# Optimization experiments

Hardware: AMD Instinct MI355X
Metric: run time of the kernel (lower is better)

## Reference

```python
import jax, jax.numpy as jnp
import numpy as np

EPS = 1e-6


def _cosine(mem, keys):
    # mem: [B,N,C], keys: [B,C,R] -> [B,N,R]
    dot = jnp.einsum('bnc,bcr->bnr', mem, keys)
    mn = jnp.linalg.norm(mem, axis=2, keepdims=True)      # [B,N,1]
    kn = jnp.linalg.norm(keys, axis=1, keepdims=True)     # [B,1,R]
    return dot / (mn * kn + EPS)


def setup_inputs() -> dict:
    B, N, C, R = 8, 2048, 256, 4
    key = jax.random.key(0)
    ks = jax.random.split(key, 16)
    return {
        'memory': jax.random.normal(ks[0], (B, N, C), jnp.float32),
        'link': jax.random.uniform(ks[1], (B, N, N), jnp.float32),
        'usage': jax.random.uniform(ks[2], (B, N), jnp.float32),
        'read_weights': jax.random.uniform(ks[3], (B, N, R), jnp.float32),
        'write_weight_prev': jax.random.uniform(ks[4], (B, N), jnp.float32),
        'precedence': jax.random.uniform(ks[5], (B, N), jnp.float32),
        'read_keys': jax.random.normal(ks[6], (B, C, R), jnp.float32),
        'read_strengths': jax.random.uniform(ks[7], (B, R), jnp.float32),
        'write_key': jax.random.normal(ks[8], (B, C), jnp.float32),
        'write_strength': jax.random.uniform(ks[9], (B, 1), jnp.float32),
        'free_gates': jax.random.uniform(ks[10], (B, R), jnp.float32),
        'allocation_gate': jax.random.uniform(ks[11], (B, 1), jnp.float32),
        'write_gate': jax.random.uniform(ks[12], (B, 1), jnp.float32),
        'write_vector': jax.random.normal(ks[13], (B, C), jnp.float32),
        'erase_vector': jax.random.uniform(ks[14], (B, C), jnp.float32),
        'read_modes': jax.random.uniform(ks[15], (B, 3, R), jnp.float32),
    }


def reference(memory, link, usage, read_weights, write_weight_prev, precedence,
              read_keys, read_strengths, write_key, write_strength, free_gates,
              allocation_gate, write_gate, write_vector, erase_vector, read_modes):
    B, N, C = memory.shape
    # --- usage update: psi retention from free gates ---
    psi = jnp.prod(1.0 - free_gates[:, None, :] * read_weights, axis=2)  # [B,N]
    u = (usage + write_weight_prev - usage * write_weight_prev) * psi
    # --- allocation weighting (sorted exclusive cumprod) ---
    order = jnp.argsort(u, axis=1)                                     # ascending usage
    u_sorted = jnp.take_along_axis(u, order, axis=1)
    excl = jnp.concatenate([jnp.ones_like(u_sorted[:, :1]),
                            jnp.cumprod(u_sorted[:, :-1], axis=1)], axis=1)
    a_sorted = (1.0 - u_sorted) * excl
    inv = jnp.argsort(order, axis=1)
    alloc = jnp.take_along_axis(a_sorted, inv, axis=1)                 # [B,N]
    # --- write weighting ---
    phi_w = _cosine(memory, write_key[:, :, None])[:, :, 0]            # [B,N]
    cw = jax.nn.softmax(phi_w * write_strength, axis=1)
    ww = write_gate * (allocation_gate * alloc + (1.0 - allocation_gate) * cw)  # [B,N]
    # --- memory write (erase + add) ---
    mem_new = memory * (1.0 - ww[:, :, None] * erase_vector[:, None, :]) \
              + ww[:, :, None] * write_vector[:, None, :]
    # --- precedence + link matrix ---
    prec_new = (1.0 - jnp.sum(ww, axis=1, keepdims=True)) * precedence + ww
    link_new = (1.0 - ww[:, :, None] - ww[:, None, :]) * link \
               + ww[:, :, None] * precedence[:, None, :]
    link_new = link_new * (1.0 - jnp.eye(N, dtype=link.dtype))[None]
    # --- directional weightings ---
    fwd = jnp.einsum('bij,bjr->bir', link_new, read_weights)           # [B,N,R]
    bwd = jnp.einsum('bji,bjr->bir', link_new, read_weights)
    # --- content read weighting on updated memory ---
    phi_r = _cosine(mem_new, read_keys)                                # [B,N,R]
    cr = jax.nn.softmax(phi_r * read_strengths[:, None, :], axis=1)
    rw_new = read_modes[:, 0][:, None, :] * bwd \
             + read_modes[:, 1][:, None, :] * cr \
             + read_modes[:, 2][:, None, :] * fwd                      # [B,N,R]
    # --- read vectors ---
    read_vectors = jnp.einsum('bnc,bnr->bcr', mem_new, rw_new)         # [B,C,R]
    return read_vectors
```

## Files before the change

### kernel.cpp

```cpp
#include <hip/hip_runtime.h>
#include <math.h>

#define EPS 1e-6f
constexpr int B = 8, N = 2048, C = 256, R = 4;

__device__ __forceinline__ float wred_sum(float v) {
  for (int d = 32; d; d >>= 1) v += __shfl_xor(v, d, 64);
  return v;
}

__device__ __forceinline__ float ww_inline(float sw, float al, float dw,
                                           float agv, float wgv) {
  return wgv * (agv * al + (1.f - agv) * (expf(sw) / dw));
}

__global__ __launch_bounds__(1024) void k_pre(const float* __restrict__ usage,
    const float* __restrict__ wwp, const float* __restrict__ fg,
    const float* __restrict__ rw, const float* __restrict__ mem,
    const float* __restrict__ wk, const float* __restrict__ wstr,
    float* __restrict__ alloc_, float* __restrict__ sw_, float* __restrict__ denw) {
  __shared__ float2 ulg[N];
  __shared__ float Sp[16][64];
  __shared__ float eacc[16];
  int blk = blockIdx.x;
  int t = threadIdx.x;
  if (blk < 256) {
    int b = blk >> 5, chunk = blk & 31;
    float gx = fg[b * R + 0], gy = fg[b * R + 1], gz = fg[b * R + 2], gw2 = fg[b * R + 3];
    for (int e = t; e < N; e += 1024) {
      float4 r4 = *(const float4*)&rw[(size_t)(b * N + e) * R];
      float psi = (1.f - gx * r4.x) * (1.f - gy * r4.y) * (1.f - gz * r4.z) * (1.f - gw2 * r4.w);
      float us = usage[b * N + e], w = wwp[b * N + e];
      float u = (us + w - us * w) * psi;
      ulg[e] = make_float2(u, log2f(u));
    }
    __syncthreads();
    int i = chunk * 64 + (t & 63);
    int jseg = t >> 6;
    float ui = ulg[i].x;
    float S = 0.f;
    int j0 = jseg * 128;
    #pragma unroll 4
    for (int jj = 0; jj < 128; jj++) {
      int j = j0 + jj;
      float2 v = ulg[j];
      bool sel = (v.x < ui) || (v.x == ui && j < i);
      S += sel ? v.y : 0.f;
    }
    Sp[jseg][t & 63] = S;
    __syncthreads();
    if (t < 64) {
      float tot = 0.f;
      #pragma unroll
      for (int s = 0; s < 16; s++) tot += Sp[s][t];
      int ii = chunk * 64 + t;
      alloc_[b * N + ii] = (1.f - ulg[ii].x) * exp2f(tot);
    }
  } else {
    int wv = t >> 6, lane = t & 63;
    int gw = (blk - 256) * 16 + wv;
    int b = gw >> 11, n = gw & (N - 1);
    float4 m4 = *(const float4*)&mem[(size_t)(b * N + n) * C + lane * 4];
    float4 k4 = *(const float4*)&wk[b * C + lane * 4];
    float dot = m4.x * k4.x + m4.y * k4.y + m4.z * k4.z + m4.w * k4.w;
    float nrm = m4.x * m4.x + m4.y * m4.y + m4.z * m4.z + m4.w * m4.w;
    float knr = k4.x * k4.x + k4.y * k4.y + k4.z * k4.z + k4.w * k4.w;
    for (int d = 32; d; d >>= 1) {
      dot += __shfl_xor(dot, d, 64);
      nrm += __shfl_xor(nrm, d, 64);
      knr += __shfl_xor(knr, d, 64);
    }
    if (lane == 0) {
      float phi = dot / (sqrtf(nrm) * sqrtf(knr) + EPS);
      float swv = phi * wstr[b];
      sw_[b * N + n] = swv;
      eacc[wv] = expf(swv);
    }
    __syncthreads();
    if (t == 0) {
      float s = 0.f;
      #pragma unroll
      for (int i = 0; i < 16; i++) s += eacc[i];
      atomicAdd(&denw[b], s);
    }
  }
}

__global__ __launch_bounds__(512) void k_mid(const float* __restrict__ link,
    const float* __restrict__ rw, const float* __restrict__ sw_,
    const float* __restrict__ alloc_, const float* __restrict__ denw,
    const float* __restrict__ ag, const float* __restrict__ wg,
    const float* __restrict__ prec, const float* __restrict__ mem,
    const float* __restrict__ rk, const float* __restrict__ ev,
    const float* __restrict__ wvec, const float* __restrict__ rs,
    float* __restrict__ t_, float* __restrict__ upart, float* __restrict__ sr_,
    float* __restrict__ denr, float* __restrict__ ST_) {
  __shared__ float tred[64][8][8];
  __shared__ float eacc[8][4];
  __shared__ float red8[8][8];
  const int blk = blockIdx.x;
  const int t = threadIdx.x;
  const int lane = t & 63, wv = t >> 6;
  if (blk < 256) {
    const int b = blk >> 5;
    const int strip = blk & 31;
    const int i0 = strip * 64;
    const int jb = t * 4;
    const float agv = ag[b], wgv = wg[b], dw = denw[b];
    float cw[4][8];
    {
      float4 sw4 = *(const float4*)&sw_[b * N + jb];
      float4 al4 = *(const float4*)&alloc_[b * N + jb];
      float wj[4] = { ww_inline(sw4.x, al4.x, dw, agv, wgv),
                      ww_inline(sw4.y, al4.y, dw, agv, wgv),
                      ww_inline(sw4.z, al4.z, dw, agv, wgv),
                      ww_inline(sw4.w, al4.w, dw, agv, wgv) };
      #pragma unroll
      for (int k = 0; k < 4; k++) {
        float4 r4 = *(const float4*)&rw[(size_t)(b * N + jb + k) * R];
        cw[k][0] = r4.x; cw[k][1] = r4.y; cw[k][2] = r4.z; cw[k][3] = r4.w;
        cw[k][4] = wj[k] * r4.x; cw[k][5] = wj[k] * r4.y;
        cw[k][6] = wj[k] * r4.z; cw[k][7] = wj[k] * r4.w;
      }
    }
    float uacc[4][8];
    #pragma unroll
    for (int k = 0; k < 4; k++) {
      #pragma unroll
      for (int r = 0; r < 8; r++) uacc[k][r] = 0.f;
    }
    const float* Lbase = link + (size_t)(b * N + i0) * N;
    for (int ii = 0; ii < 64; ii += 4) {
      float4 La[4];
      #pragma unroll
      for (int m = 0; m < 4; m++)
        La[m] = *(const float4*)(Lbase + (size_t)(ii + m) * N + jb);
      #pragma unroll
      for (int m = 0; m < 4; m++) {
        const int i = i0 + ii + m;
        float4 q = *(const float4*)&rw[(size_t)(b * N + i) * R];
        float wi = ww_inline(sw_[b * N + i], alloc_[b * N + i], dw, agv, wgv);
        float ri[8] = { q.x, q.y, q.z, q.w, wi * q.x, wi * q.y, wi * q.z, wi * q.w };
        float lv[4] = { La[m].x, La[m].y, La[m].z, La[m].w };
        float trow[8] = { 0, 0, 0, 0, 0, 0, 0, 0 };
        #pragma unroll
        for (int k = 0; k < 4; k++) {
          #pragma unroll
          for (int r = 0; r < 8; r++) {
            uacc[k][r] = fmaf(lv[k], ri[r], uacc[k][r]);
            trow[r] = fmaf(lv[k], cw[k][r], trow[r]);
          }
        }
        float nv[4];
        #pragma unroll
        for (int rr = 0; rr < 4; rr++) {
          float a = trow[2 * rr], c = trow[2 * rr + 1];
          float oa = __shfl_xor(a, 1, 64), oc = __shfl_xor(c, 1, 64);
          nv[rr] = (lane & 1) ? (c + oc) : (a + oa);
        }
        float nw[2];
        #pragma unroll
        for (int rr = 0; rr < 2; rr++) {
          float a = nv[2 * rr], c = nv[2 * rr + 1];
          float oa = __shfl_xor(a, 2, 64), oc = __shfl_xor(c, 2, 64);
          nw[rr] = (lane & 2) ? (c + oc) : (a + oa);
        }
        float a2 = nw[0], c2 = nw[1];
        float oa2 = __shfl_xor(a2, 4, 64), oc2 = __shfl_xor(c2, 4, 64);
        float vv = (lane & 4) ? (c2 + oc2) : (a2 + oa2);
        vv += __shfl_xor(vv, 8, 64);
        vv += __shfl_xor(vv, 16, 64);
        vv += __shfl_xor(vv, 32, 64);
        if (lane < 8) tred[ii + m][wv][lane] = vv;
      }
    }
    __syncthreads();
    {
      int i = t & 63, r = t >> 6;
      float s = 0.f;
      #pragma unroll
      for (int w8 = 0; w8 < 8; w8++) s += tred[i][w8][r];
      t_[((size_t)(b * 8 + r)) * N + i0 + i] = s;
    }
    float* ub = upart + ((size_t)(b * 32 + strip) * 8) * N;
    #pragma unroll
    for (int r = 0; r < 8; r++) {
      float4 v = { uacc[0][r], uacc[1][r], uacc[2][r], uacc[3][r] };
      *(float4*)(ub + (size_t)r * N + jb) = v;
    }
  } else if (blk < 2304) {
    int gw = (blk - 256) * 8 + wv;
    int b = gw >> 11, n = gw & (N - 1);
    const float agv = ag[b], wgv = wg[b], dw = denw[b];
    float w = ww_inline(sw_[b * N + n], alloc_[b * N + n], dw, agv, wgv);
    int c0 = lane * 4;
    float4 m4 = *(const float4*)&mem[(size_t)(b * N + n) * C + c0];
    float4 e4 = *(const float4*)&ev[b * C + c0];
    float4 v4 = *(const float4*)&wvec[b * C + c0];
    float mn[4] = { m4.x * (1.f - w * e4.x) + w * v4.x,
                    m4.y * (1.f - w * e4.y) + w * v4.y,
                    m4.z * (1.f - w * e4.z) + w * v4.z,
                    m4.w * (1.f - w * e4.w) + w * v4.w };
    float dot[4] = { 0, 0, 0, 0 };
    float kn[4] = { 0, 0, 0, 0 };
    float nrm = 0.f;
    #pragma unroll
    for (int ci = 0; ci < 4; ci++) {
      float4 k4 = *(const float4*)&rk[(size_t)(b * C + c0 + ci) * R];
      dot[0] = fmaf(mn[ci], k4.x, dot[0]);
      dot[1] = fmaf(mn[ci], k4.y, dot[1]);
      dot[2] = fmaf(mn[ci], k4.z, dot[2]);
      dot[3] = fmaf(mn[ci], k4.w, dot[3]);
      kn[0] = fmaf(k4.x, k4.x, kn[0]);
      kn[1] = fmaf(k4.y, k4.y, kn[1]);
      kn[2] = fmaf(k4.z, k4.z, kn[2]);
      kn[3] = fmaf(k4.w, k4.w, kn[3]);
      nrm = fmaf(mn[ci], mn[ci], nrm);
    }
    for (int d = 32; d; d >>= 1) {
      dot[0] += __shfl_xor(dot[0], d, 64);
      dot[1] += __shfl_xor(dot[1], d, 64);
      dot[2] += __shfl_xor(dot[2], d, 64);
      dot[3] += __shfl_xor(dot[3], d, 64);
      kn[0] += __shfl_xor(kn[0], d, 64);
      kn[1] += __shfl_xor(kn[1], d, 64);
      kn[2] += __shfl_xor(kn[2], d, 64);
      kn[3] += __shfl_xor(kn[3], d, 64);
      nrm += __shfl_xor(nrm, d, 64);
    }
    if (lane == 0) {
      float mnorm = sqrtf(nrm);
      #pragma unroll
      for (int r = 0; r < 4; r++) {
        float phi = dot[r] / (mnorm * sqrtf(kn[r]) + EPS);
        float sv = phi * rs[b * R + r];
        sr_[(size_t)(b * R + r) * N + n] = sv;
        eacc[wv][r] = expf(sv);
      }
    }
    __syncthreads();
    if (t < 4) {
      float s = 0.f;
      #pragma unroll
      for (int i = 0; i < 8; i++) s += eacc[i][t];
      atomicAdd(&denr[b * R + t], s);
    }
  } else {
    int b = blk - 2304;
    const float agv = ag[b], wgv = wg[b], dw = denw[b];
    float a[8] = { 0, 0, 0, 0, 0, 0, 0, 0 };
    #pragma unroll
    for (int k = 0; k < 4; k++) {
      int i = t + k * 512;
      float4 r4 = *(const float4*)&rw[(size_t)(b * N + i) * R];
      float pc = prec[b * N + i];
      float w = ww_inline(sw_[b * N + i], alloc_[b * N + i], dw, agv, wgv);
      a[0] = fmaf(pc, r4.x, a[0]); a[1] = fmaf(pc, r4.y, a[1]);
      a[2] = fmaf(pc, r4.z, a[2]); a[3] = fmaf(pc, r4.w, a[3]);
      a[4] = fmaf(w, r4.x, a[4]);  a[5] = fmaf(w, r4.y, a[5]);
      a[6] = fmaf(w, r4.z, a[6]);  a[7] = fmaf(w, r4.w, a[7]);
    }
    #pragma unroll
    for (int r = 0; r < 8; r++) a[r] = wred_sum(a[r]);
    if (lane == 0) {
      #pragma unroll
      for (int r = 0; r < 8; r++) red8[wv][r] = a[r];
    }
    __syncthreads();
    if (t < 8) {
      float s = 0.f;
      #pragma unroll
      for (int i = 0; i < 8; i++) s += red8[i][t];
      ST_[b * 8 + t] = s;
    }
  }
}

__global__ __launch_bounds__(256) void k_combread(const float* __restrict__ link,
    const float* __restrict__ sw_, const float* __restrict__ alloc_,
    const float* __restrict__ denw, const float* __restrict__ denr,
    const float* __restrict__ ag, const float* __restrict__ wg,
    const float* __restrict__ prec, const float* __restrict__ rw,
    const float* __restrict__ t_, const float* __restrict__ upart,
    const float* __restrict__ sr_, const float* __restrict__ ST_,
    const float* __restrict__ modes, const float* __restrict__ mem,
    const float* __restrict__ ev, const float* __restrict__ wvec,
    float* __restrict__ part_) {
  __shared__ float dgl[64], wloc[64], rwnl[4][64];
  __shared__ float red[4][64][4][4];
  const int blk = blockIdx.x;
  const int b = blk >> 5, chunk = blk & 31;
  const int n0 = chunk * 64;
  const int t = threadIdx.x;
  const int nl = t & 63, r = t >> 6;
  const int n = n0 + nl;
  const float agv = ag[b], wgv = wg[b], dw = denw[b];
  float u1 = 0.f, u2 = 0.f;
  const float* up = upart + ((size_t)(b * 32) * 8) * N;
  #pragma unroll 8
  for (int s = 0; s < 32; s++) {
    const float* p = up + ((size_t)s * 8) * N;
    u1 += p[(size_t)r * N + n];
    u2 += p[(size_t)(4 + r) * N + n];
  }
  float pc = prec[b * N + n];
  if (r == 0) {
    float w = ww_inline(sw_[b * N + n], alloc_[b * N + n], dw, agv, wgv);
    float L = link[((size_t)(b * N + n)) * N + n];
    dgl[nl] = (1.f - 2.f * w) * L + w * pc;
    wloc[nl] = w;
  }
  __syncthreads();
  {
    float w = wloc[nl], Dg = dgl[nl];
    float t1 = t_[(size_t)(b * 8 + r) * N + n];
    float t2 = t_[(size_t)(b * 8 + 4 + r) * N + n];
    float sv = sr_[(size_t)(b * R + r) * N + n];
    float cr = expf(sv) / denr[b * R + r];
    float rv = rw[(size_t)(b * N + n) * R + r];
    float S = ST_[b * 8 + r], T = ST_[b * 8 + 4 + r];
    float m0 = modes[(b * 3 + 0) * R + r], m1 = modes[(b * 3 + 1) * R + r],
          m2 = modes[(b * 3 + 2) * R + r];
    float fwd = (1.f - w) * t1 - t2 + w * S - Dg * rv;
    float bwd = (1.f - w) * u1 - u2 + pc * T - Dg * rv;
    rwnl[r][nl] = m0 * bwd + m1 * cr + m2 * fwd;
  }
  __syncthreads();
  const int sub = r, cg = nl;
  const int c0 = cg * 4;
  float4 e4 = *(const float4*)&ev[b * C + c0];
  float4 v4 = *(const float4*)&wvec[b * C + c0];
  float acc[4][4];
  #pragma unroll
  for (int ci = 0; ci < 4; ci++) {
    #pragma unroll
    for (int rr = 0; rr < 4; rr++) acc[ci][rr] = 0.f;
  }
  for (int m = 0; m < 16; m++) {
    int row = sub * 16 + m;
    int nn = n0 + row;
    float w = wloc[row];
    float4 m4 = *(const float4*)&mem[(size_t)(b * N + nn) * C + c0];
    float mn[4] = { m4.x * (1.f - w * e4.x) + w * v4.x,
                    m4.y * (1.f - w * e4.y) + w * v4.y,
                    m4.z * (1.f - w * e4.z) + w * v4.z,
                    m4.w * (1.f - w * e4.w) + w * v4.w };
    float rv[4] = { rwnl[0][row], rwnl[1][row], rwnl[2][row], rwnl[3][row] };
    #pragma unroll
    for (int ci = 0; ci < 4; ci++) {
      #pragma unroll
      for (int rr = 0; rr < 4; rr++) acc[ci][rr] = fmaf(mn[ci], rv[rr], acc[ci][rr]);
    }
  }
  #pragma unroll
  for (int ci = 0; ci < 4; ci++) {
    #pragma unroll
    for (int rr = 0; rr < 4; rr++) red[sub][cg][ci][rr] = acc[ci][rr];
  }
  __syncthreads();
  if (sub == 0) {
    #pragma unroll
    for (int ci = 0; ci < 4; ci++) {
      #pragma unroll
      for (int rr = 0; rr < 4; rr++) {
        float s = red[0][cg][ci][rr] + red[1][cg][ci][rr] +
                  red[2][cg][ci][rr] + red[3][cg][ci][rr];
        part_[((size_t)blk * C + (c0 + ci)) * R + rr] = s;
      }
    }
  }
}

__global__ void k_final(const float* __restrict__ part_, float* __restrict__ out) {
  int idx = blockIdx.x * 256 + threadIdx.x;
  if (idx >= B * C * R) return;
  int b = idx / (C * R), cr = idx % (C * R);
  float s = 0.f;
  for (int ch = 0; ch < 32; ch++) s += part_[(size_t)(b * 32 + ch) * C * R + cr];
  out[idx] = s;
}

extern "C" void kernel_launch(void* const* d_in, const int* in_sizes, int n_in,
                              void* d_out, int out_size, void* d_ws, size_t ws_size,
                              hipStream_t stream) {
  const float* mem   = (const float*)d_in[0];
  const float* link  = (const float*)d_in[1];
  const float* usage = (const float*)d_in[2];
  const float* rw    = (const float*)d_in[3];
  const float* wwp   = (const float*)d_in[4];
  const float* prec  = (const float*)d_in[5];
  const float* rk    = (const float*)d_in[6];
  const float* rs    = (const float*)d_in[7];
  const float* wk    = (const float*)d_in[8];
  const float* wstr  = (const float*)d_in[9];
  const float* fg    = (const float*)d_in[10];
  const float* ag    = (const float*)d_in[11];
  const float* wg    = (const float*)d_in[12];
  const float* wvec  = (const float*)d_in[13];
  const float* ev    = (const float*)d_in[14];
  const float* modes = (const float*)d_in[15];
  float* out = (float*)d_out;

  float* W = (float*)d_ws;
  float* denw  = W;
  float* denr  = W + 8;
  float* alloc_= W + 64;
  float* sw_   = alloc_ + B * N;
  float* ST_   = sw_ + B * N;
  float* t_    = ST_ + 64;
  float* sr_   = t_ + B * 8 * N;
  float* part_ = sr_ + B * R * N;
  float* upart = part_ + B * 32 * C * R;

  (void)hipMemsetAsync(W, 0, 64 * sizeof(float), stream);
  k_pre<<<256 + (B * N) / 16, 1024, 0, stream>>>(usage, wwp, fg, rw, mem, wk, wstr,
                                                 alloc_, sw_, denw);
  k_mid<<<256 + (B * N) / 8 + B, 512, 0, stream>>>(link, rw, sw_, alloc_, denw, ag, wg,
                                                   prec, mem, rk, ev, wvec, rs,
                                                   t_, upart, sr_, denr, ST_);
  k_combread<<<B * 32, 256, 0, stream>>>(link, sw_, alloc_, denw, denr, ag, wg, prec,
                                         rw, t_, upart, sr_, ST_, modes, mem, ev,
                                         wvec, part_);
  k_final<<<(B * C * R) / 256, 256, 0, stream>>>(part_, out);
}
```

Measured before the change: 111.4 us.

## Split link strips into 32-row blocks and stage row coefficients in LDS

```diff
diff --git a/kernel.cpp b/kernel.cpp
--- a/kernel.cpp
+++ b/kernel.cpp
@@ -86,7 +86,7 @@
   }
 }
 
-__global__ __launch_bounds__(512) void k_mid(const float* __restrict__ link,
+__global__ __launch_bounds__(512, 4) void k_mid(const float* __restrict__ link,
     const float* __restrict__ rw, const float* __restrict__ sw_,
     const float* __restrict__ alloc_, const float* __restrict__ denw,
     const float* __restrict__ ag, const float* __restrict__ wg,
@@ -95,18 +95,26 @@
     const float* __restrict__ wvec, const float* __restrict__ rs,
     float* __restrict__ t_, float* __restrict__ upart, float* __restrict__ sr_,
     float* __restrict__ denr, float* __restrict__ ST_) {
-  __shared__ float tred[64][8][8];
+  __shared__ float tred[32][8][8];
+  __shared__ float ri8[32][8];
   __shared__ float eacc[8][4];
   __shared__ float red8[8][8];
   const int blk = blockIdx.x;
   const int t = threadIdx.x;
   const int lane = t & 63, wv = t >> 6;
-  if (blk < 256) {
-    const int b = blk >> 5;
-    const int strip = blk & 31;
-    const int i0 = strip * 64;
+  if (blk < 512) {
+    const int b = blk >> 6;
+    const int strip = blk & 63;
+    const int i0 = strip * 32;
     const int jb = t * 4;
     const float agv = ag[b], wgv = wg[b], dw = denw[b];
+    if (t < 32) {
+      int i = i0 + t;
+      float4 q = *(const float4*)&rw[(size_t)(b * N + i) * R];
+      float wi = ww_inline(sw_[b * N + i], alloc_[b * N + i], dw, agv, wgv);
+      ri8[t][0] = q.x; ri8[t][1] = q.y; ri8[t][2] = q.z; ri8[t][3] = q.w;
+      ri8[t][4] = wi * q.x; ri8[t][5] = wi * q.y; ri8[t][6] = wi * q.z; ri8[t][7] = wi * q.w;
+    }
     float cw[4][8];
     {
       float4 sw4 = *(const float4*)&sw_[b * N + jb];
@@ -129,67 +137,82 @@
       #pragma unroll
       for (int r = 0; r < 8; r++) uacc[k][r] = 0.f;
     }
+    __syncthreads();
     const float* Lbase = link + (size_t)(b * N + i0) * N;
-    for (int ii = 0; ii < 64; ii += 4) {
-      float4 La[4];
-      #pragma unroll
-      for (int m = 0; m < 4; m++)
-        La[m] = *(const float4*)(Lbase + (size_t)(ii + m) * N + jb);
-      #pragma unroll
-      for (int m = 0; m < 4; m++) {
-        const int i = i0 + ii + m;
-        float4 q = *(const float4*)&rw[(size_t)(b * N + i) * R];
-        float wi = ww_inline(sw_[b * N + i], alloc_[b * N + i], dw, agv, wgv);
-        float ri[8] = { q.x, q.y, q.z, q.w, wi * q.x, wi * q.y, wi * q.z, wi * q.w };
-        float lv[4] = { La[m].x, La[m].y, La[m].z, La[m].w };
-        float trow[8] = { 0, 0, 0, 0, 0, 0, 0, 0 };
+    for (int ii = 0; ii < 32; ii += 2) {
+      float4 La[2];
+      La[0] = *(const float4*)(Lbase + (size_t)(ii + 0) * N + jb);
+      La[1] = *(const float4*)(Lbase + (size_t)(ii + 1) * N + jb);
+      float trow[2][8];
+      #pragma unroll
+      for (int p = 0; p < 2; p++) {
+        float lv[4] = { La[p].x, La[p].y, La[p].z, La[p].w };
+        float ri[8];
+        #pragma unroll
+        for (int r = 0; r < 8; r++) { ri[r] = ri8[ii + p][r]; trow[p][r] = 0.f; }
         #pragma unroll
         for (int k = 0; k < 4; k++) {
           #pragma unroll
           for (int r = 0; r < 8; r++) {
             uacc[k][r] = fmaf(lv[k], ri[r], uacc[k][r]);
-            trow[r] = fmaf(lv[k], cw[k][r], trow[r]);
+            trow[p][r] = fmaf(lv[k], cw[k][r], trow[p][r]);
           }
         }
-        float nv[4];
+      }
+      float nv[2][4];
+      #pragma unroll
+      for (int p = 0; p < 2; p++) {
         #pragma unroll
         for (int rr = 0; rr < 4; rr++) {
-          float a = trow[2 * rr], c = trow[2 * rr + 1];
+          float a = trow[p][2 * rr], c = trow[p][2 * rr + 1];
           float oa = __shfl_xor(a, 1, 64), oc = __shfl_xor(c, 1, 64);
-          nv[rr] = (lane & 1) ? (c + oc) : (a + oa);
+          nv[p][rr] = (lane & 1) ? (c + oc) : (a + oa);
         }
-        float nw[2];
+      }
+      float nw[2][2];
+      #pragma unroll
+      for (int p = 0; p < 2; p++) {
         #pragma unroll
         for (int rr = 0; rr < 2; rr++) {
-          float a = nv[2 * rr], c = nv[2 * rr + 1];
+          float a = nv[p][2 * rr], c = nv[p][2 * rr + 1];
           float oa = __shfl_xor(a, 2, 64), oc = __shfl_xor(c, 2, 64);
-          nw[rr] = (lane & 2) ? (c + oc) : (a + oa);
+          nw[p][rr] = (lane & 2) ? (c + oc) : (a + oa);
         }
-        float a2 = nw[0], c2 = nw[1];
+      }
+      float vv[2];
+      #pragma unroll
+      for (int p = 0; p < 2; p++) {
+        float a2 = nw[p][0], c2 = nw[p][1];
         float oa2 = __shfl_xor(a2, 4, 64), oc2 = __shfl_xor(c2, 4, 64);
-        float vv = (lane & 4) ? (c2 + oc2) : (a2 + oa2);
-        vv += __shfl_xor(vv, 8, 64);
-        vv += __shfl_xor(vv, 16, 64);
-        vv += __shfl_xor(vv, 32, 64);
-        if (lane < 8) tred[ii + m][wv][lane] = vv;
-      }
-    }
-    __syncthreads();
-    {
-      int i = t & 63, r = t >> 6;
+        vv[p] = (lane & 4) ? (c2 + oc2) : (a2 + oa2);
+      }
+      #pragma unroll
+      for (int p = 0; p < 2; p++) vv[p] += __shfl_xor(vv[p], 8, 64);
+      #pragma unroll
+      for (int p = 0; p < 2; p++) vv[p] += __shfl_xor(vv[p], 16, 64);
+      #pragma unroll
+      for (int p = 0; p < 2; p++) vv[p] += __shfl_xor(vv[p], 32, 64);
+      if (lane < 8) {
+        tred[ii + 0][wv][lane] = vv[0];
+        tred[ii + 1][wv][lane] = vv[1];
+      }
+    }
+    __syncthreads();
+    if (t < 256) {
+      int i = t >> 3, r = t & 7;
       float s = 0.f;
       #pragma unroll
       for (int w8 = 0; w8 < 8; w8++) s += tred[i][w8][r];
       t_[((size_t)(b * 8 + r)) * N + i0 + i] = s;
     }
-    float* ub = upart + ((size_t)(b * 32 + strip) * 8) * N;
+    float* ub = upart + ((size_t)(b * 64 + strip) * 8) * N;
     #pragma unroll
     for (int r = 0; r < 8; r++) {
       float4 v = { uacc[0][r], uacc[1][r], uacc[2][r], uacc[3][r] };
       *(float4*)(ub + (size_t)r * N + jb) = v;
     }
-  } else if (blk < 2304) {
-    int gw = (blk - 256) * 8 + wv;
+  } else if (blk < 2560) {
+    int gw = (blk - 512) * 8 + wv;
     int b = gw >> 11, n = gw & (N - 1);
     const float agv = ag[b], wgv = wg[b], dw = denw[b];
     float w = ww_inline(sw_[b * N + n], alloc_[b * N + n], dw, agv, wgv);
@@ -246,7 +269,7 @@
       atomicAdd(&denr[b * R + t], s);
     }
   } else {
-    int b = blk - 2304;
+    int b = blk - 2560;
     const float agv = ag[b], wgv = wg[b], dw = denw[b];
     float a[8] = { 0, 0, 0, 0, 0, 0, 0, 0 };
     #pragma unroll
@@ -296,9 +319,9 @@
   const int n = n0 + nl;
   const float agv = ag[b], wgv = wg[b], dw = denw[b];
   float u1 = 0.f, u2 = 0.f;
-  const float* up = upart + ((size_t)(b * 32) * 8) * N;
+  const float* up = upart + ((size_t)(b * 64) * 8) * N;
   #pragma unroll 8
-  for (int s = 0; s < 32; s++) {
+  for (int s = 0; s < 64; s++) {
     const float* p = up + ((size_t)s * 8) * N;
     u1 += p[(size_t)r * N + n];
     u2 += p[(size_t)(4 + r) * N + n];
@@ -415,7 +438,7 @@
   (void)hipMemsetAsync(W, 0, 64 * sizeof(float), stream);
   k_pre<<<256 + (B * N) / 16, 1024, 0, stream>>>(usage, wwp, fg, rw, mem, wk, wstr,
                                                  alloc_, sw_, denw);
-  k_mid<<<256 + (B * N) / 8 + B, 512, 0, stream>>>(link, rw, sw_, alloc_, denw, ag, wg,
+  k_mid<<<512 + (B * N) / 8 + B, 512, 0, stream>>>(link, rw, sw_, alloc_, denw, ag, wg,
                                                    prec, mem, rk, ev, wvec, rs,
                                                    t_, upart, sr_, denr, ST_);
   k_combread<<<B * 32, 256, 0, stream>>>(link, sw_, alloc_, denw, denr, ag, wg, prec,
```

After: 136.0 us. +22.1%, slower.

## Double-buffer link row loads and precompute per-row read weights in shared memory

Applied to the files above, without the earlier changes.

```diff
diff --git a/kernel.cpp b/kernel.cpp
--- a/kernel.cpp
+++ b/kernel.cpp
@@ -86,6 +86,58 @@
   }
 }
 
+#define LOADM(buf, rbase)                                                     \
+  {                                                                           \
+    _Pragma("unroll") for (int m = 0; m < 8; m++)                             \
+        buf[m] = *(const float4*)(Lbase + (size_t)((rbase) + m) * N + jb);    \
+  }
+
+#define PROC4(buf, off, rbase)                                                \
+  {                                                                           \
+    float trow[4][8];                                                         \
+    _Pragma("unroll") for (int p = 0; p < 4; p++) {                           \
+      const int lr_ = (rbase) - i0 + (off) + p;                               \
+      float lv[4] = { buf[(off) + p].x, buf[(off) + p].y,                     \
+                      buf[(off) + p].z, buf[(off) + p].w };                   \
+      _Pragma("unroll") for (int r = 0; r < 8; r++) trow[p][r] = 0.f;         \
+      _Pragma("unroll") for (int k = 0; k < 4; k++) {                         \
+        _Pragma("unroll") for (int r = 0; r < 8; r++) {                       \
+          uacc[k][r] = fmaf(lv[k], ri8[lr_][r], uacc[k][r]);                  \
+          trow[p][r] = fmaf(lv[k], cw[k][r], trow[p][r]);                     \
+        }                                                                     \
+      }                                                                       \
+    }                                                                         \
+    float nv[4][4];                                                           \
+    _Pragma("unroll") for (int p = 0; p < 4; p++) {                           \
+      _Pragma("unroll") for (int rr = 0; rr < 4; rr++) {                      \
+        float a = trow[p][2 * rr], c = trow[p][2 * rr + 1];                   \
+        float oa = __shfl_xor(a, 1, 64), oc = __shfl_xor(c, 1, 64);           \
+        nv[p][rr] = (lane & 1) ? (c + oc) : (a + oa);                         \
+      }                                                                       \
+    }                                                                         \
+    float nw2[4][2];                                                          \
+    _Pragma("unroll") for (int p = 0; p < 4; p++) {                           \
+      _Pragma("unroll") for (int rr = 0; rr < 2; rr++) {                      \
+        float a = nv[p][2 * rr], c = nv[p][2 * rr + 1];                       \
+        float oa = __shfl_xor(a, 2, 64), oc = __shfl_xor(c, 2, 64);           \
+        nw2[p][rr] = (lane & 2) ? (c + oc) : (a + oa);                        \
+      }                                                                       \
+    }                                                                         \
+    float vv[4];                                                              \
+    _Pragma("unroll") for (int p = 0; p < 4; p++) {                           \
+      float a2 = nw2[p][0], c2 = nw2[p][1];                                   \
+      float oa2 = __shfl_xor(a2, 4, 64), oc2 = __shfl_xor(c2, 4, 64);         \
+      vv[p] = (lane & 4) ? (c2 + oc2) : (a2 + oa2);                           \
+    }                                                                         \
+    _Pragma("unroll") for (int p = 0; p < 4; p++) vv[p] += __shfl_xor(vv[p], 8, 64);  \
+    _Pragma("unroll") for (int p = 0; p < 4; p++) vv[p] += __shfl_xor(vv[p], 16, 64); \
+    _Pragma("unroll") for (int p = 0; p < 4; p++) vv[p] += __shfl_xor(vv[p], 32, 64); \
+    if (lane < 8) {                                                           \
+      _Pragma("unroll") for (int p = 0; p < 4; p++)                           \
+          tred[(rbase) - i0 + (off) + p][wv][lane] = vv[p];                   \
+    }                                                                         \
+  }
+
 __global__ __launch_bounds__(512) void k_mid(const float* __restrict__ link,
     const float* __restrict__ rw, const float* __restrict__ sw_,
     const float* __restrict__ alloc_, const float* __restrict__ denw,
@@ -96,6 +148,7 @@
     float* __restrict__ t_, float* __restrict__ upart, float* __restrict__ sr_,
     float* __restrict__ denr, float* __restrict__ ST_) {
   __shared__ float tred[64][8][8];
+  __shared__ float ri8[64][8];
   __shared__ float eacc[8][4];
   __shared__ float red8[8][8];
   const int blk = blockIdx.x;
@@ -107,6 +160,13 @@
     const int i0 = strip * 64;
     const int jb = t * 4;
     const float agv = ag[b], wgv = wg[b], dw = denw[b];
+    if (t < 64) {
+      int i = i0 + t;
+      float4 q = *(const float4*)&rw[(size_t)(b * N + i) * R];
+      float wi = ww_inline(sw_[b * N + i], alloc_[b * N + i], dw, agv, wgv);
+      ri8[t][0] = q.x; ri8[t][1] = q.y; ri8[t][2] = q.z; ri8[t][3] = q.w;
+      ri8[t][4] = wi * q.x; ri8[t][5] = wi * q.y; ri8[t][6] = wi * q.z; ri8[t][7] = wi * q.w;
+    }
     float cw[4][8];
     {
       float4 sw4 = *(const float4*)&sw_[b * N + jb];
@@ -129,54 +189,23 @@
       #pragma unroll
       for (int r = 0; r < 8; r++) uacc[k][r] = 0.f;
     }
-    const float* Lbase = link + (size_t)(b * N + i0) * N;
-    for (int ii = 0; ii < 64; ii += 4) {
-      float4 La[4];
-      #pragma unroll
-      for (int m = 0; m < 4; m++)
-        La[m] = *(const float4*)(Lbase + (size_t)(ii + m) * N + jb);
-      #pragma unroll
-      for (int m = 0; m < 4; m++) {
-        const int i = i0 + ii + m;
-        float4 q = *(const float4*)&rw[(size_t)(b * N + i) * R];
-        float wi = ww_inline(sw_[b * N + i], alloc_[b * N + i], dw, agv, wgv);
-        float ri[8] = { q.x, q.y, q.z, q.w, wi * q.x, wi * q.y, wi * q.z, wi * q.w };
-        float lv[4] = { La[m].x, La[m].y, La[m].z, La[m].w };
-        float trow[8] = { 0, 0, 0, 0, 0, 0, 0, 0 };
-        #pragma unroll
-        for (int k = 0; k < 4; k++) {
-          #pragma unroll
-          for (int r = 0; r < 8; r++) {
-            uacc[k][r] = fmaf(lv[k], ri[r], uacc[k][r]);
-            trow[r] = fmaf(lv[k], cw[k][r], trow[r]);
-          }
-        }
-        float nv[4];
-        #pragma unroll
-        for (int rr = 0; rr < 4; rr++) {
-          float a = trow[2 * rr], c = trow[2 * rr + 1];
-          float oa = __shfl_xor(a, 1, 64), oc = __shfl_xor(c, 1, 64);
-          nv[rr] = (lane & 1) ? (c + oc) : (a + oa);
-        }
-        float nw[2];
-        #pragma unroll
-        for (int rr = 0; rr < 2; rr++) {
-          float a = nv[2 * rr], c = nv[2 * rr + 1];
-          float oa = __shfl_xor(a, 2, 64), oc = __shfl_xor(c, 2, 64);
-          nw[rr] = (lane & 2) ? (c + oc) : (a + oa);
-        }
-        float a2 = nw[0], c2 = nw[1];
-        float oa2 = __shfl_xor(a2, 4, 64), oc2 = __shfl_xor(c2, 4, 64);
-        float vv = (lane & 4) ? (c2 + oc2) : (a2 + oa2);
-        vv += __shfl_xor(vv, 8, 64);
-        vv += __shfl_xor(vv, 16, 64);
-        vv += __shfl_xor(vv, 32, 64);
-        if (lane < 8) tred[ii + m][wv][lane] = vv;
-      }
+    __syncthreads();
+    const float* Lbase = link + (size_t)b * N * N;
+    float4 bufA[8], bufB[8];
+    LOADM(bufA, i0);
+    #pragma unroll
+    for (int g = 0; g < 4; g++) {
+      const int r0 = i0 + g * 16;
+      LOADM(bufB, r0 + 8);
+      PROC4(bufA, 0, r0);
+      PROC4(bufA, 4, r0);
+      if (g < 3) LOADM(bufA, r0 + 16);
+      PROC4(bufB, 0, r0 + 8);
+      PROC4(bufB, 4, r0 + 8);
     }
     __syncthreads();
     {
-      int i = t & 63, r = t >> 6;
+      int i = t >> 3, r = t & 7;
       float s = 0.f;
       #pragma unroll
       for (int w8 = 0; w8 < 8; w8++) s += tred[i][w8][r];
```

New measurement: 251.5 us. 2.26x slower.

## Compute link row-products via LDS-tiled double-buffered pass with precomputed coefficients

Applied to the files above, without the earlier changes.

```diff
diff --git a/kernel.cpp b/kernel.cpp
--- a/kernel.cpp
+++ b/kernel.cpp
@@ -86,18 +86,55 @@
   }
 }
 
+__global__ __launch_bounds__(512) void k_cw(const float* __restrict__ rw,
+    const float* __restrict__ sw_, const float* __restrict__ alloc_,
+    const float* __restrict__ denw, const float* __restrict__ ag,
+    const float* __restrict__ wg, const float* __restrict__ prec,
+    float* __restrict__ cwg, float* __restrict__ ST_) {
+  __shared__ float red8[8][8];
+  int blk = blockIdx.x, t = threadIdx.x;
+  int b = blk >> 2, seg = blk & 3;
+  int n = seg * 512 + t;
+  int lane = t & 63, wv = t >> 6;
+  float agv = ag[b], wgv = wg[b], dw = denw[b];
+  float4 r4 = *(const float4*)&rw[(size_t)(b * N + n) * R];
+  float w = ww_inline(sw_[b * N + n], alloc_[b * N + n], dw, agv, wgv);
+  float pc = prec[b * N + n];
+  float4 lo = { r4.x, r4.y, r4.z, r4.w };
+  float4 hi = { w * r4.x, w * r4.y, w * r4.z, w * r4.w };
+  *(float4*)&cwg[(size_t)(b * N + n) * 8] = lo;
+  *(float4*)&cwg[(size_t)(b * N + n) * 8 + 4] = hi;
+  float a[8] = { pc * r4.x, pc * r4.y, pc * r4.z, pc * r4.w,
+                 w * r4.x,  w * r4.y,  w * r4.z,  w * r4.w };
+  #pragma unroll
+  for (int r = 0; r < 8; r++) a[r] = wred_sum(a[r]);
+  if (lane == 0) {
+    #pragma unroll
+    for (int r = 0; r < 8; r++) red8[wv][r] = a[r];
+  }
+  __syncthreads();
+  if (t < 8) {
+    float s = 0.f;
+    #pragma unroll
+    for (int i = 0; i < 8; i++) s += red8[i][t];
+    atomicAdd(&ST_[b * 8 + t], s);
+  }
+}
+
 __global__ __launch_bounds__(512) void k_mid(const float* __restrict__ link,
     const float* __restrict__ rw, const float* __restrict__ sw_,
     const float* __restrict__ alloc_, const float* __restrict__ denw,
     const float* __restrict__ ag, const float* __restrict__ wg,
-    const float* __restrict__ prec, const float* __restrict__ mem,
-    const float* __restrict__ rk, const float* __restrict__ ev,
-    const float* __restrict__ wvec, const float* __restrict__ rs,
+    const float* __restrict__ mem, const float* __restrict__ rk,
+    const float* __restrict__ ev, const float* __restrict__ wvec,
+    const float* __restrict__ rs, const float* __restrict__ cwg,
     float* __restrict__ t_, float* __restrict__ upart, float* __restrict__ sr_,
-    float* __restrict__ denr, float* __restrict__ ST_) {
-  __shared__ float tred[64][8][8];
+    float* __restrict__ denr) {
+  __shared__ float tile[2][64][65];
+  __shared__ float cwt[2][64][8];
+  __shared__ float ri8l[64][8];
+  __shared__ float tred[8][64][9];
   __shared__ float eacc[8][4];
-  __shared__ float red8[8][8];
   const int blk = blockIdx.x;
   const int t = threadIdx.x;
   const int lane = t & 63, wv = t >> 6;
@@ -106,81 +143,87 @@
     const int strip = blk & 31;
     const int i0 = strip * 64;
     const int jb = t * 4;
-    const float agv = ag[b], wgv = wg[b], dw = denw[b];
-    float cw[4][8];
+    const int lr = t >> 3, lc = (t & 7) * 8;
+    const int li = t & 63, seg = t >> 6;
+    ri8l[t >> 3][t & 7] = cwg[(size_t)(b * N + i0) * 8 + t];
+    float tacc[8] = { 0, 0, 0, 0, 0, 0, 0, 0 };
+    float uacc[4][8];
+    #pragma unroll
+    for (int k = 0; k < 4; k++) {
+      #pragma unroll
+      for (int r = 0; r < 8; r++) uacc[k][r] = 0.f;
+    }
+    const float* lsrc = link + (size_t)(b * N + i0 + lr) * N + lc;
     {
-      float4 sw4 = *(const float4*)&sw_[b * N + jb];
-      float4 al4 = *(const float4*)&alloc_[b * N + jb];
-      float wj[4] = { ww_inline(sw4.x, al4.x, dw, agv, wgv),
-                      ww_inline(sw4.y, al4.y, dw, agv, wgv),
-                      ww_inline(sw4.z, al4.z, dw, agv, wgv),
-                      ww_inline(sw4.w, al4.w, dw, agv, wgv) };
-      #pragma unroll
-      for (int k = 0; k < 4; k++) {
-        float4 r4 = *(const float4*)&rw[(size_t)(b * N + jb + k) * R];
-        cw[k][0] = r4.x; cw[k][1] = r4.y; cw[k][2] = r4.z; cw[k][3] = r4.w;
-        cw[k][4] = wj[k] * r4.x; cw[k][5] = wj[k] * r4.y;
-        cw[k][6] = wj[k] * r4.z; cw[k][7] = wj[k] * r4.w;
-      }
-    }
-    float uacc[4][8];
-    #pragma unroll
-    for (int k = 0; k < 4; k++) {
-      #pragma unroll
-      for (int r = 0; r < 8; r++) uacc[k][r] = 0.f;
-    }
-    const float* Lbase = link + (size_t)(b * N + i0) * N;
+      float4 pa = *(const float4*)lsrc;
+      float4 pb = *(const float4*)(lsrc + 4);
+      float cwreg = cwg[(size_t)(b * N) * 8 + t];
+      tile[0][lr][lc + 0] = pa.x; tile[0][lr][lc + 1] = pa.y;
+      tile[0][lr][lc + 2] = pa.z; tile[0][lr][lc + 3] = pa.w;
+      tile[0][lr][lc + 4] = pb.x; tile[0][lr][lc + 5] = pb.y;
+      tile[0][lr][lc + 6] = pb.z; tile[0][lr][lc + 7] = pb.w;
+      cwt[0][t >> 3][t & 7] = cwreg;
+    }
+    __syncthreads();
+    for (int T = 0; T < 32; T++) {
+      const int cur = T & 1;
+      float4 pa, pb;
+      float cwreg;
+      if (T < 31) {
+        pa = *(const float4*)(lsrc + (size_t)(T + 1) * 64);
+        pb = *(const float4*)(lsrc + (size_t)(T + 1) * 64 + 4);
+        cwreg = cwg[(size_t)(b * N + (T + 1) * 64) * 8 + t];
+      }
+      #pragma unroll
+      for (int jj = 0; jj < 8; jj++) {
+        int j = seg * 8 + jj;
+        float lv = tile[cur][li][j];
+        float4 c0 = *(const float4*)&cwt[cur][j][0];
+        float4 c1 = *(const float4*)&cwt[cur][j][4];
+        tacc[0] = fmaf(lv, c0.x, tacc[0]);
+        tacc[1] = fmaf(lv, c0.y, tacc[1]);
+        tacc[2] = fmaf(lv, c0.z, tacc[2]);
+        tacc[3] = fmaf(lv, c0.w, tacc[3]);
+        tacc[4] = fmaf(lv, c1.x, tacc[4]);
+        tacc[5] = fmaf(lv, c1.y, tacc[5]);
+        tacc[6] = fmaf(lv, c1.z, tacc[6]);
+        tacc[7] = fmaf(lv, c1.w, tacc[7]);
+      }
+      if (T < 31) {
+        const int nb = cur ^ 1;
+        tile[nb][lr][lc + 0] = pa.x; tile[nb][lr][lc + 1] = pa.y;
+        tile[nb][lr][lc + 2] = pa.z; tile[nb][lr][lc + 3] = pa.w;
+        tile[nb][lr][lc + 4] = pb.x; tile[nb][lr][lc + 5] = pb.y;
+        tile[nb][lr][lc + 6] = pb.z; tile[nb][lr][lc + 7] = pb.w;
+        cwt[nb][t >> 3][t & 7] = cwreg;
+      }
+      __syncthreads();
+    }
     for (int ii = 0; ii < 64; ii += 4) {
       float4 La[4];
       #pragma unroll
       for (int m = 0; m < 4; m++)
-        La[m] = *(const float4*)(Lbase + (size_t)(ii + m) * N + jb);
+        La[m] = *(const float4*)(link + (size_t)(b * N + i0 + ii + m) * N + jb);
       #pragma unroll
       for (int m = 0; m < 4; m++) {
-        const int i = i0 + ii + m;
-        float4 q = *(const float4*)&rw[(size_t)(b * N + i) * R];
-        float wi = ww_inline(sw_[b * N + i], alloc_[b * N + i], dw, agv, wgv);
-        float ri[8] = { q.x, q.y, q.z, q.w, wi * q.x, wi * q.y, wi * q.z, wi * q.w };
         float lv[4] = { La[m].x, La[m].y, La[m].z, La[m].w };
-        float trow[8] = { 0, 0, 0, 0, 0, 0, 0, 0 };
         #pragma unroll
         for (int k = 0; k < 4; k++) {
           #pragma unroll
-          for (int r = 0; r < 8; r++) {
-            uacc[k][r] = fmaf(lv[k], ri[r], uacc[k][r]);
-            trow[r] = fmaf(lv[k], cw[k][r], trow[r]);
-          }
+          for (int r = 0; r < 8; r++)
+            uacc[k][r] = fmaf(lv[k], ri8l[ii + m][r], uacc[k][r]);
         }
-        float nv[4];
-        #pragma unroll
-        for (int rr = 0; rr < 4; rr++) {
-          float a = trow[2 * rr], c = trow[2 * rr + 1];
-          float oa = __shfl_xor(a, 1, 64), oc = __shfl_xor(c, 1, 64);
-          nv[rr] = (lane & 1) ? (c + oc) : (a + oa);
-        }
-        float nw[2];
-        #pragma unroll
-        for (int rr = 0; rr < 2; rr++) {
-          float a = nv[2 * rr], c = nv[2 * rr + 1];
-          float oa = __shfl_xor(a, 2, 64), oc = __shfl_xor(c, 2, 64);
-          nw[rr] = (lane & 2) ? (c + oc) : (a + oa);
-        }
-        float a2 = nw[0], c2 = nw[1];
-        float oa2 = __shfl_xor(a2, 4, 64), oc2 = __shfl_xor(c2, 4, 64);
-        float vv = (lane & 4) ? (c2 + oc2) : (a2 + oa2);
-        vv += __shfl_xor(vv, 8, 64);
-        vv += __shfl_xor(vv, 16, 64);
-        vv += __shfl_xor(vv, 32, 64);
-        if (lane < 8) tred[ii + m][wv][lane] = vv;
-      }
-    }
+      }
+    }
+    #pragma unroll
+    for (int r = 0; r < 8; r++) tred[seg][li][r] = tacc[r];
     __syncthreads();
     {
-      int i = t & 63, r = t >> 6;
+      const int i = t & 63, rr = t >> 6;
       float s = 0.f;
       #pragma unroll
-      for (int w8 = 0; w8 < 8; w8++) s += tred[i][w8][r];
-      t_[((size_t)(b * 8 + r)) * N + i0 + i] = s;
+      for (int sg = 0; sg < 8; sg++) s += tred[sg][i][rr];
+      t_[((size_t)(b * 8 + rr)) * N + i0 + i] = s;
     }
     float* ub = upart + ((size_t)(b * 32 + strip) * 8) * N;
     #pragma unroll
@@ -188,15 +231,15 @@
       float4 v = { uacc[0][r], uacc[1][r], uacc[2][r], uacc[3][r] };
       *(float4*)(ub + (size_t)r * N + jb) = v;
     }
-  } else if (blk < 2304) {
+  } else {
     int gw = (blk - 256) * 8 + wv;
     int b = gw >> 11, n = gw & (N - 1);
     const float agv = ag[b], wgv = wg[b], dw = denw[b];
     float w = ww_inline(sw_[b * N + n], alloc_[b * N + n], dw, agv, wgv);
-    int c0 = lane * 4;
-    float4 m4 = *(const float4*)&mem[(size_t)(b * N + n) * C + c0];
-    float4 e4 = *(const float4*)&ev[b * C + c0];
-    float4 v4 = *(const float4*)&wvec[b * C + c0];
+    int c0i = lane * 4;
+    float4 m4 = *(const float4*)&mem[(size_t)(b * N + n) * C + c0i];
+    float4 e4 = *(const float4*)&ev[b * C + c0i];
+    float4 v4 = *(const float4*)&wvec[b * C + c0i];
     float mn[4] = { m4.x * (1.f - w * e4.x) + w * v4.x,
                     m4.y * (1.f - w * e4.y) + w * v4.y,
                     m4.z * (1.f - w * e4.z) + w * v4.z,
@@ -206,7 +249,7 @@
     float nrm = 0.f;
     #pragma unroll
     for (int ci = 0; ci < 4; ci++) {
-      float4 k4 = *(const float4*)&rk[(size_t)(b * C + c0 + ci) * R];
+      float4 k4 = *(const float4*)&rk[(size_t)(b * C + c0i + ci) * R];
       dot[0] = fmaf(mn[ci], k4.x, dot[0]);
       dot[1] = fmaf(mn[ci], k4.y, dot[1]);
       dot[2] = fmaf(mn[ci], k4.z, dot[2]);
@@ -244,34 +287,6 @@
       #pragma unroll
       for (int i = 0; i < 8; i++) s += eacc[i][t];
       atomicAdd(&denr[b * R + t], s);
-    }
-  } else {
-    int b = blk - 2304;
-    const float agv = ag[b], wgv = wg[b], dw = denw[b];
-    float a[8] = { 0, 0, 0, 0, 0, 0, 0, 0 };
-    #pragma unroll
-    for (int k = 0; k < 4; k++) {
-      int i = t + k * 512;
-      float4 r4 = *(const float4*)&rw[(size_t)(b * N + i) * R];
-      float pc = prec[b * N + i];
-      float w = ww_inline(sw_[b * N + i], alloc_[b * N + i], dw, agv, wgv);
-      a[0] = fmaf(pc, r4.x, a[0]); a[1] = fmaf(pc, r4.y, a[1]);
-      a[2] = fmaf(pc, r4.z, a[2]); a[3] = fmaf(pc, r4.w, a[3]);
-      a[4] = fmaf(w, r4.x, a[4]);  a[5] = fmaf(w, r4.y, a[5]);
-      a[6] = fmaf(w, r4.z, a[6]);  a[7] = fmaf(w, r4.w, a[7]);
-    }
-    #pragma unroll
-    for (int r = 0; r < 8; r++) a[r] = wred_sum(a[r]);
-    if (lane == 0) {
-      #pragma unroll
-      for (int r = 0; r < 8; r++) red8[wv][r] = a[r];
-    }
-    __syncthreads();
-    if (t < 8) {
-      float s = 0.f;
-      #pragma unroll
-      for (int i = 0; i < 8; i++) s += red8[i][t];
-      ST_[b * 8 + t] = s;
     }
   }
 }
@@ -404,20 +419,22 @@
   float* W = (float*)d_ws;
   float* denw  = W;
   float* denr  = W + 8;
-  float* alloc_= W + 64;
+  float* ST_   = W + 64;
+  float* alloc_= W + 128;
   float* sw_   = alloc_ + B * N;
-  float* ST_   = sw_ + B * N;
-  float* t_    = ST_ + 64;
+  float* t_    = sw_ + B * N;
   float* sr_   = t_ + B * 8 * N;
   float* part_ = sr_ + B * R * N;
-  float* upart = part_ + B * 32 * C * R;
-
-  (void)hipMemsetAsync(W, 0, 64 * sizeof(float), stream);
+  float* cwg   = part_ + B * 32 * C * R;
+  float* upart = cwg + B * N * 8;
+
+  (void)hipMemsetAsync(W, 0, 128 * sizeof(float), stream);
   k_pre<<<256 + (B * N) / 16, 1024, 0, stream>>>(usage, wwp, fg, rw, mem, wk, wstr,
                                                  alloc_, sw_, denw);
-  k_mid<<<256 + (B * N) / 8 + B, 512, 0, stream>>>(link, rw, sw_, alloc_, denw, ag, wg,
-                                                   prec, mem, rk, ev, wvec, rs,
-                                                   t_, upart, sr_, denr, ST_);
+  k_cw<<<B * 4, 512, 0, stream>>>(rw, sw_, alloc_, denw, ag, wg, prec, cwg, ST_);
+  k_mid<<<256 + (B * N) / 8, 512, 0, stream>>>(link, rw, sw_, alloc_, denw, ag, wg,
+                                               mem, rk, ev, wvec, rs, cwg,
+                                               t_, upart, sr_, denr);
   k_combread<<<B * 32, 256, 0, stream>>>(link, sw_, alloc_, denw, denr, ag, wg, prec,
                                          rw, t_, upart, sr_, ST_, modes, mem, ev,
                                          wvec, part_);
```

After: 137.5 us. +23.4%, slower.
